# Kernel tuning notes

Hardware: AMD Instinct MI355X
Metric: run time of the kernel (lower is better)

## Reference

```python
import jax, jax.numpy as jnp
import numpy as np

B, T, C, H = 4, 4096, 1024, 64

def setup_inputs() -> dict:
    key = jax.random.key(0)
    kx, kq, kk, kv = jax.random.split(key, 4)
    x = jax.random.normal(kx, (B, T, C), dtype=jnp.float32)
    Wq = jax.random.normal(kq, (C, H), dtype=jnp.float32) * (C ** -0.5)
    Wk = jax.random.normal(kk, (C, H), dtype=jnp.float32) * (C ** -0.5)
    Wv = jax.random.normal(kv, (C, H), dtype=jnp.float32) * (C ** -0.5)
    return {"x": x, "Wq": Wq, "Wk": Wk, "Wv": Wv}

def reference(x, Wq, Wk, Wv):
    # single-head causal attention, dropout p=0 (eval)
    q = jnp.einsum('btc,ch->bth', x, Wq)  # [B,T,H]
    k = jnp.einsum('btc,ch->bth', x, Wk)
    v = jnp.einsum('btc,ch->bth', x, Wv)
    scale = k.shape[-1] ** -0.5
    scores = jnp.einsum('bth,bsh->bts', q, k) * scale  # [B,T,T]
    causal = jnp.tril(jnp.ones((q.shape[1], q.shape[1]), dtype=bool))
    scores = jnp.where(causal, scores, -jnp.inf)
    weights = jax.nn.softmax(scores, axis=-1)
    out = jnp.einsum('bts,bsh->bth', weights, v)  # [B,T,H]
    return out
```

## Files before the change

kernel.cpp:

```cpp
#include <hip/hip_runtime.h>


typedef short  s16x8 __attribute__((ext_vector_type(8)));
typedef float  f32x4 __attribute__((ext_vector_type(4)));

constexpr int B = 4, T = 4096, C = 1024, H = 64;
constexpr int M = B * T;
constexpr float LOG2E = 1.44269504088896340736f;
constexpr float QSCALE = 0.125f * LOG2E;
constexpr float MBASE  = 4.0f * LOG2E;

__device__ __forceinline__ unsigned short f2bf(float f) {
    union { float f; unsigned u; } v; v.f = f;
    unsigned r = v.u + 0x7fffu + ((v.u >> 16) & 1u);
    return (unsigned short)(r >> 16);
}

__device__ __forceinline__ unsigned cvt_pk_bf16(float lo, float hi) {
    unsigned r;
    asm("v_cvt_pk_bf16_f32 %0, %1, %2" : "=v"(r) : "v"(lo), "v"(hi));
    return r;
}

__device__ __forceinline__ void gl_lds16(const void* g, void* l) {
    __builtin_amdgcn_global_load_lds(
        (const __attribute__((address_space(1))) unsigned*)g,
        (__attribute__((address_space(3))) unsigned*)l, 16, 0, 0);
}

__global__ void prep_w(const float* __restrict__ Wq, const float* __restrict__ Wk,
                       const float* __restrict__ Wv, unsigned short* __restrict__ Wt) {
    const int n = blockIdx.x;
    const float* W = (n < 64) ? Wq : (n < 128 ? Wk : Wv);
    const int col = n & 63;
    for (int k = threadIdx.x; k < C; k += blockDim.x)
        Wt[(size_t)n * C + k] = f2bf(W[(size_t)k * H + col]);
}

__global__ __launch_bounds__(512) void qkv_proj(
    const float* __restrict__ x, const unsigned short* __restrict__ Wt,
    unsigned short* __restrict__ Q, unsigned short* __restrict__ K,
    unsigned short* __restrict__ V) {
    __shared__ __align__(16) unsigned short ldsA[2][32 * 64];
    __shared__ __align__(16) unsigned short ldsB[2][192 * 64];

    const int t = threadIdx.x, lane = t & 63, w = t >> 6;
    const int i = lane & 15, g = lane >> 4;
    const int rowbase = blockIdx.x * 32;
    const int rw = w & 1, nw = w >> 1;

    const int arow = t >> 3, aslot = t & 7;
    const float* aga = x + (size_t)(rowbase + arow) * C + ((aslot ^ (arow & 7)) * 8);
    const int awoff = arow * 64 + aslot * 8;
    const bool astage = (t < 256);

    const int brow8 = lane >> 3, bslot = lane & 7;
    const unsigned short* bga[3];
    int bn0[3];
#pragma unroll
    for (int j = 0; j < 3; ++j) {
        bn0[j] = w * 24 + j * 8;
        bga[j] = Wt + (size_t)(bn0[j] + brow8) * C + ((bslot ^ brow8) * 8);
    }

    f32x4 acc[3];
#pragma unroll
    for (int n = 0; n < 3; ++n) acc[n] = (f32x4){0.f, 0.f, 0.f, 0.f};

    {
#pragma unroll
        for (int j = 0; j < 3; ++j)
            gl_lds16(bga[j], &ldsB[0][bn0[j] * 64]);
        if (astage) {
            f32x4 a0 = *(const f32x4*)(aga);
            f32x4 a1 = *(const f32x4*)(aga + 4);
            union { unsigned u[4]; s16x8 v; } av;
            av.u[0] = cvt_pk_bf16(a0[0], a0[1]);
            av.u[1] = cvt_pk_bf16(a0[2], a0[3]);
            av.u[2] = cvt_pk_bf16(a1[0], a1[1]);
            av.u[3] = cvt_pk_bf16(a1[2], a1[3]);
            *(s16x8*)&ldsA[0][awoff] = av.v;
        }
    }
    __syncthreads();

    for (int it = 0; it < 16; ++it) {
        const int cur = it & 1, nxt = cur ^ 1;
        const int kc = (it + 1) * 64;
        f32x4 a0, a1;
        const bool more = (it < 15);
        if (more) {
            if (astage) {
                a0 = *(const f32x4*)(aga + kc);
                a1 = *(const f32x4*)(aga + kc + 4);
            }
#pragma unroll
            for (int j = 0; j < 3; ++j)
                gl_lds16(bga[j] + kc, &ldsB[nxt][bn0[j] * 64]);
        }
#pragma unroll
        for (int kst = 0; kst < 2; ++kst) {
            const int c = kst * 4 + g;
            s16x8 a = *(const s16x8*)&ldsA[cur][(rw * 16 + i) * 64 + ((c ^ (i & 7)) * 8)];
#pragma unroll
            for (int nt = 0; nt < 3; ++nt) {
                int n = nw * 48 + nt * 16 + i;
                s16x8 b = *(const s16x8*)&ldsB[cur][n * 64 + ((c ^ (i & 7)) * 8)];
                acc[nt] = __builtin_amdgcn_mfma_f32_16x16x32_bf16(a, b, acc[nt], 0, 0, 0);
            }
        }
        if (more && astage) {
            union { unsigned u[4]; s16x8 v; } av;
            av.u[0] = cvt_pk_bf16(a0[0], a0[1]);
            av.u[1] = cvt_pk_bf16(a0[2], a0[3]);
            av.u[2] = cvt_pk_bf16(a1[0], a1[1]);
            av.u[3] = cvt_pk_bf16(a1[2], a1[3]);
            *(s16x8*)&ldsA[nxt][awoff] = av.v;
        }
        __syncthreads();
    }

#pragma unroll
    for (int nt = 0; nt < 3; ++nt) {
        int n = nw * 48 + nt * 16 + i;
#pragma unroll
        for (int r = 0; r < 4; ++r) {
            int row = rowbase + rw * 16 + g * 4 + r;
            float val = acc[nt][r];
            if (n < 64)       Q[(size_t)row * H + n]         = f2bf(val * QSCALE);
            else if (n < 128) K[(size_t)row * H + (n - 64)]  = f2bf(val);
            else              V[(size_t)row * H + (n - 128)] = f2bf(val);
        }
    }
}

__global__ __launch_bounds__(256) void vtrans(const unsigned short* __restrict__ V,
                                              unsigned short* __restrict__ VT) {
    __shared__ __align__(16) unsigned short tile[64][72];
    const int b = blockIdx.x >> 6, t0 = (blockIdx.x & 63) * 64;
    const int tid = threadIdx.x;
    {
        int row = tid >> 2, col = (tid & 3) * 16;
        s16x8 v0 = *(const s16x8*)(V + (size_t)(b * T + t0 + row) * H + col);
        s16x8 v1 = *(const s16x8*)(V + (size_t)(b * T + t0 + row) * H + col + 8);
        *(s16x8*)&tile[row][col]     = v0;
        *(s16x8*)&tile[row][col + 8] = v1;
    }
    __syncthreads();
    {
        int h = tid >> 2, tcol = (tid & 3) * 16;
        s16x8 o0, o1;
#pragma unroll
        for (int j = 0; j < 8; ++j) {
            int pos = tcol + j, c = pos >> 5, pp = pos & 31;
            int tok = (c << 5) | (((pp >> 2) & 1) << 4) | ((pp >> 3) << 2) | (pp & 3);
            o0[j] = (short)tile[tok][h];
        }
#pragma unroll
        for (int j = 0; j < 8; ++j) {
            int pos = tcol + 8 + j, c = pos >> 5, pp = pos & 31;
            int tok = (c << 5) | (((pp >> 2) & 1) << 4) | ((pp >> 3) << 2) | (pp & 3);
            o1[j] = (short)tile[tok][h];
        }
        unsigned short* dst = VT + (size_t)(b * H + h) * T + t0 + tcol;
        *(s16x8*)dst       = o0;
        *(s16x8*)(dst + 8) = o1;
    }
}

__global__ __launch_bounds__(256) void attn(
    const unsigned short* __restrict__ Qg, const unsigned short* __restrict__ Kg,
    const unsigned short* __restrict__ VTg,
    float* __restrict__ Opart, float* __restrict__ lpart) {
    __shared__ __align__(16) unsigned short ks[2][64 * 64];
    __shared__ __align__(16) unsigned short vs[2][64 * 64];

    const int t = threadIdx.x, lane = t & 63, w = t >> 6;
    const int bid = blockIdx.x;
    const int xcd3 = bid & 7;
    const int b = xcd3 >> 1, s0 = xcd3 & 1;
    const int rest = bid >> 3;
    const int qgi = rest >> 1, s1 = rest & 1;
    const int sp = s1 * 2 + s0;
    const int qg = 63 - qgi;
    const int q0w = qg * 64 + w * 16;
    const int i = lane & 15, g = lane >> 4, g4 = g * 4;
    const int nkv = qg + 1;

    const unsigned short* Kb = Kg  + (size_t)b * T * H;
    const unsigned short* Vb = VTg + (size_t)b * H * T;

    const int r8 = lane >> 3, sl = lane & 7, sx = sl ^ r8;

    const unsigned short* Qrow = Qg + (size_t)(b * T + q0w + i) * H;
    s16x8 bq0 = *(const s16x8*)(Qrow + g * 8);
    s16x8 bq1 = *(const s16x8*)(Qrow + 32 + g * 8);

    f32x4 oacc[4];
#pragma unroll
    for (int nt = 0; nt < 4; ++nt) oacc[nt] = (f32x4){0.f, 0.f, 0.f, 0.f};
    float l_run = 0.f;

    if (sp < nkv) {
        const int kv0 = sp * 64;
#pragma unroll
        for (int j = 0; j < 2; ++j) {
            const int row = (w + j * 4) * 8 + r8;
            gl_lds16(Kb + (size_t)(kv0 + row) * H + sx * 8, &ks[0][row * 64 + sl * 8]);
            gl_lds16(Vb + (size_t)row * T + kv0 + sx * 8,   &vs[0][row * 64 + sl * 8]);
        }
    }
    __syncthreads();

    int cur = 0;
    for (int tile = sp; tile < nkv; tile += 4) {
        const int kv = tile * 64;
        if (tile + 4 < nkv) {
            const int kvn = kv + 256;
#pragma unroll
            for (int j = 0; j < 2; ++j) {
                const int row = (w + j * 4) * 8 + r8;
                gl_lds16(Kb + (size_t)(kvn + row) * H + sx * 8, &ks[cur ^ 1][row * 64 + sl * 8]);
                gl_lds16(Vb + (size_t)row * T + kvn + sx * 8,   &vs[cur ^ 1][row * 64 + sl * 8]);
            }
        }

        s16x8 kb[8], vb[8];
#pragma unroll
        for (int kst = 0; kst < 2; ++kst)
#pragma unroll
            for (int nt = 0; nt < 4; ++nt) {
                const int off = (nt * 16 + i) * 64 + (((kst * 4 + g) ^ (i & 7)) * 8);
                kb[kst * 4 + nt] = *(const s16x8*)&ks[cur][off];
                vb[kst * 4 + nt] = *(const s16x8*)&vs[cur][off];
            }

        f32x4 s[4];
#pragma unroll
        for (int nt = 0; nt < 4; ++nt)
            s[nt] = (f32x4){-MBASE, -MBASE, -MBASE, -MBASE};
#pragma unroll
        for (int nt = 0; nt < 4; ++nt)
            s[nt] = __builtin_amdgcn_mfma_f32_16x16x32_bf16(kb[nt], bq0, s[nt], 0, 0, 0);
#pragma unroll
        for (int nt = 0; nt < 4; ++nt)
            s[nt] = __builtin_amdgcn_mfma_f32_16x16x32_bf16(kb[4 + nt], bq1, s[nt], 0, 0, 0);

        if (kv + 63 > q0w) {
            const int thr = q0w + i - kv;
#pragma unroll
            for (int nt = 0; nt < 4; ++nt)
#pragma unroll
                for (int r = 0; r < 4; ++r)
                    if (nt * 16 + g4 + r > thr) s[nt][r] = -INFINITY;
        }

#pragma unroll
        for (int nt = 0; nt < 4; ++nt)
#pragma unroll
            for (int r = 0; r < 4; ++r)
                s[nt][r] = exp2f(s[nt][r]);

#pragma unroll
        for (int kst = 0; kst < 2; ++kst) {
            union { unsigned u[4]; s16x8 v; } pb;
            pb.u[0] = cvt_pk_bf16(s[2 * kst][0],     s[2 * kst][1]);
            pb.u[1] = cvt_pk_bf16(s[2 * kst][2],     s[2 * kst][3]);
            pb.u[2] = cvt_pk_bf16(s[2 * kst + 1][0], s[2 * kst + 1][1]);
            pb.u[3] = cvt_pk_bf16(s[2 * kst + 1][2], s[2 * kst + 1][3]);
#pragma unroll
            for (int nt = 0; nt < 4; ++nt)
                oacc[nt] = __builtin_amdgcn_mfma_f32_16x16x32_bf16(vb[kst * 4 + nt], pb.v, oacc[nt], 0, 0, 0);
        }

        l_run += ((s[0][0] + s[0][1]) + (s[0][2] + s[0][3]))
               + ((s[1][0] + s[1][1]) + (s[1][2] + s[1][3]))
               + ((s[2][0] + s[2][1]) + (s[2][2] + s[2][3]))
               + ((s[3][0] + s[3][1]) + (s[3][2] + s[3][3]));

        __syncthreads();
        cur ^= 1;
    }

    l_run += __shfl_xor(l_run, 16);
    l_run += __shfl_xor(l_run, 32);
#pragma unroll
    for (int nt = 0; nt < 4; ++nt)
        *(f32x4*)&Opart[((size_t)bid * 64 + w * 16 + i) * 64 + nt * 16 + g4] = oacc[nt];
    if (g == 0) lpart[(size_t)bid * 64 + w * 16 + i] = l_run;
}

__global__ __launch_bounds__(256) void merge4(
    const float* __restrict__ Opart, const float* __restrict__ lpart,
    float* __restrict__ out) {
    const int idx = blockIdx.x * 256 + threadIdx.x;
    const int row = idx >> 4, c4 = (idx & 15) * 4;
    const int b = row >> 12, q = row & 4095;
    const int qg = q >> 6, r = q & 63;
    const int qgi = 63 - qg;

    float L = 0.f;
    f32x4 o = (f32x4){0.f, 0.f, 0.f, 0.f};
#pragma unroll
    for (int s = 0; s < 4; ++s) {
        const int bidp = ((qgi * 2 + (s >> 1)) << 3) + b * 2 + (s & 1);
        L += lpart[(size_t)bidp * 64 + r];
        f32x4 ov = *(const f32x4*)&Opart[((size_t)bidp * 64 + r) * 64 + c4];
        o[0] += ov[0]; o[1] += ov[1]; o[2] += ov[2]; o[3] += ov[3];
    }
    const float inv = 1.0f / L;
    f32x4 res = (f32x4){o[0] * inv, o[1] * inv, o[2] * inv, o[3] * inv};
    *(f32x4*)&out[(size_t)row * 64 + c4] = res;
}

extern "C" void kernel_launch(void* const* d_in, const int* in_sizes, int n_in,
                              void* d_out, int out_size, void* d_ws, size_t ws_size,
                              hipStream_t stream) {
    (void)in_sizes; (void)n_in; (void)out_size; (void)ws_size;
    const float* x  = (const float*)d_in[0];
    const float* Wq = (const float*)d_in[1];
    const float* Wk = (const float*)d_in[2];
    const float* Wv = (const float*)d_in[3];
    float* out = (float*)d_out;

    char* ws = (char*)d_ws;
    unsigned short* Q  = (unsigned short*)(ws);
    unsigned short* K  = (unsigned short*)(ws + (size_t)1 * M * H * 2);
    unsigned short* V  = (unsigned short*)(ws + (size_t)2 * M * H * 2);
    unsigned short* VT = (unsigned short*)(ws + (size_t)3 * M * H * 2);
    unsigned short* Wt = (unsigned short*)(ws + (size_t)4 * M * H * 2);
    float* Opart = (float*)(ws + (size_t)4 * M * H * 2 + 512 * 1024);
    float* lpart = (float*)(ws + (size_t)4 * M * H * 2 + 512 * 1024
                            + (size_t)1024 * 64 * 64 * 4);

    prep_w<<<192, 256, 0, stream>>>(Wq, Wk, Wv, Wt);
    qkv_proj<<<M / 32, 512, 0, stream>>>(x, Wt, Q, K, V);
    vtrans<<<B * (T / 64), 256, 0, stream>>>(V, VT);
    attn<<<1024, 256, 0, stream>>>(Q, K, VT, Opart, lpart);
    merge4<<<1024, 256, 0, stream>>>(Opart, lpart, out);
}
```

Measured before the change: 55.76 us.

## Use 128-row query tiles with 8-way KV split and bf16 partial outputs

The attention kernel now runs 512-thread blocks covering 128 query rows, so each K/V tile staged in LDS is shared by 8 waves instead of 4. The KV dimension is split 8 ways instead of 4, and waves skip tiles that lie entirely above their causal diagonal. Partial outputs are stored as bf16 instead of fp32, which halves the traffic between the attention and merge kernels. The merge now reads eight partials per row, and the bf16 partials lose some precision before normalization.

```diff
diff --git a/kernel.cpp b/kernel.cpp
--- a/kernel.cpp
+++ b/kernel.cpp
@@ -3,6 +3,7 @@
 
 typedef short  s16x8 __attribute__((ext_vector_type(8)));
 typedef float  f32x4 __attribute__((ext_vector_type(4)));
+typedef unsigned u32x2 __attribute__((ext_vector_type(2)));
 
 constexpr int B = 4, T = 4096, C = 1024, H = 64;
 constexpr int M = B * T;
@@ -168,29 +169,30 @@
     }
 }
 
-__global__ __launch_bounds__(256) void attn(
+__global__ __launch_bounds__(512, 4) void attn(
     const unsigned short* __restrict__ Qg, const unsigned short* __restrict__ Kg,
     const unsigned short* __restrict__ VTg,
-    float* __restrict__ Opart, float* __restrict__ lpart) {
+    unsigned short* __restrict__ Opb, float* __restrict__ lpart) {
     __shared__ __align__(16) unsigned short ks[2][64 * 64];
     __shared__ __align__(16) unsigned short vs[2][64 * 64];
 
     const int t = threadIdx.x, lane = t & 63, w = t >> 6;
     const int bid = blockIdx.x;
-    const int xcd3 = bid & 7;
-    const int b = xcd3 >> 1, s0 = xcd3 & 1;
-    const int rest = bid >> 3;
-    const int qgi = rest >> 1, s1 = rest & 1;
-    const int sp = s1 * 2 + s0;
-    const int qg = 63 - qgi;
-    const int q0w = qg * 64 + w * 16;
+    const int b = bid & 3;
+    const int sp = (bid >> 2) & 7;
+    const int qt = 31 - (bid >> 5);
+    const int q0 = qt * 128;
+    const int q0w = q0 + w * 16;
     const int i = lane & 15, g = lane >> 4, g4 = g * 4;
-    const int nkv = qg + 1;
+    const int nkv = 2 * qt + 2;
 
     const unsigned short* Kb = Kg  + (size_t)b * T * H;
     const unsigned short* Vb = VTg + (size_t)b * H * T;
 
-    const int r8 = lane >> 3, sl = lane & 7, sx = sl ^ r8;
+    const int srow = t >> 3, sl = t & 7, sx = sl ^ (srow & 7);
+    const unsigned short* kga = Kb + (size_t)srow * H + sx * 8;
+    const unsigned short* vga = Vb + (size_t)srow * T + sx * 8;
+    const int soff = srow * 64 + sl * 8;
 
     const unsigned short* Qrow = Qg + (size_t)(b * T + q0w + i) * H;
     s16x8 bq0 = *(const s16x8*)(Qrow + g * 8);
@@ -202,81 +204,75 @@
     float l_run = 0.f;
 
     if (sp < nkv) {
-        const int kv0 = sp * 64;
-#pragma unroll
-        for (int j = 0; j < 2; ++j) {
-            const int row = (w + j * 4) * 8 + r8;
-            gl_lds16(Kb + (size_t)(kv0 + row) * H + sx * 8, &ks[0][row * 64 + sl * 8]);
-            gl_lds16(Vb + (size_t)row * T + kv0 + sx * 8,   &vs[0][row * 64 + sl * 8]);
-        }
+        const size_t kv0 = (size_t)sp * 64;
+        gl_lds16(kga + kv0 * H, &ks[0][soff]);
+        gl_lds16(vga + kv0,     &vs[0][soff]);
     }
     __syncthreads();
 
     int cur = 0;
-    for (int tile = sp; tile < nkv; tile += 4) {
+    for (int tile = sp; tile < nkv; tile += 8) {
         const int kv = tile * 64;
-        if (tile + 4 < nkv) {
-            const int kvn = kv + 256;
-#pragma unroll
-            for (int j = 0; j < 2; ++j) {
-                const int row = (w + j * 4) * 8 + r8;
-                gl_lds16(Kb + (size_t)(kvn + row) * H + sx * 8, &ks[cur ^ 1][row * 64 + sl * 8]);
-                gl_lds16(Vb + (size_t)row * T + kvn + sx * 8,   &vs[cur ^ 1][row * 64 + sl * 8]);
+        if (tile + 8 < nkv) {
+            const size_t kvn = (size_t)kv + 512;
+            gl_lds16(kga + kvn * H, &ks[cur ^ 1][soff]);
+            gl_lds16(vga + kvn,     &vs[cur ^ 1][soff]);
+        }
+
+        if (kv <= q0w + 15) {
+            s16x8 kb[8], vb[8];
+#pragma unroll
+            for (int kst = 0; kst < 2; ++kst)
+#pragma unroll
+                for (int nt = 0; nt < 4; ++nt) {
+                    const int off = (nt * 16 + i) * 64 + (((kst * 4 + g) ^ (i & 7)) * 8);
+                    kb[kst * 4 + nt] = *(const s16x8*)&ks[cur][off];
+                    vb[kst * 4 + nt] = *(const s16x8*)&vs[cur][off];
+                }
+
+            f32x4 s[4];
+#pragma unroll
+            for (int nt = 0; nt < 4; ++nt)
+                s[nt] = (f32x4){-MBASE, -MBASE, -MBASE, -MBASE};
+#pragma unroll
+            for (int nt = 0; nt < 4; ++nt)
+                s[nt] = __builtin_amdgcn_mfma_f32_16x16x32_bf16(kb[nt], bq0, s[nt], 0, 0, 0);
+#pragma unroll
+            for (int nt = 0; nt < 4; ++nt)
+                s[nt] = __builtin_amdgcn_mfma_f32_16x16x32_bf16(kb[4 + nt], bq1, s[nt], 0, 0, 0);
+
+            if (kv + 63 > q0w) {
+                const int thr = q0w + i - kv;
+#pragma unroll
+                for (int nt = 0; nt < 4; ++nt)
+#pragma unroll
+                    for (int r = 0; r < 4; ++r)
+                        if (nt * 16 + g4 + r > thr) s[nt][r] = -INFINITY;
             }
-        }
-
-        s16x8 kb[8], vb[8];
-#pragma unroll
-        for (int kst = 0; kst < 2; ++kst)
-#pragma unroll
-            for (int nt = 0; nt < 4; ++nt) {
-                const int off = (nt * 16 + i) * 64 + (((kst * 4 + g) ^ (i & 7)) * 8);
-                kb[kst * 4 + nt] = *(const s16x8*)&ks[cur][off];
-                vb[kst * 4 + nt] = *(const s16x8*)&vs[cur][off];
+
+#pragma unroll
+            for (int nt = 0; nt < 4; ++nt)
+#pragma unroll
+                for (int r = 0; r < 4; ++r)
+                    s[nt][r] = exp2f(s[nt][r]);
+
+#pragma unroll
+            for (int kst = 0; kst < 2; ++kst) {
+                union { unsigned u[4]; s16x8 v; } pb;
+                pb.u[0] = cvt_pk_bf16(s[2 * kst][0],     s[2 * kst][1]);
+                pb.u[1] = cvt_pk_bf16(s[2 * kst][2],     s[2 * kst][3]);
+                pb.u[2] = cvt_pk_bf16(s[2 * kst + 1][0], s[2 * kst + 1][1]);
+                pb.u[3] = cvt_pk_bf16(s[2 * kst + 1][2], s[2 * kst + 1][3]);
+#pragma unroll
+                for (int nt = 0; nt < 4; ++nt)
+                    oacc[nt] = __builtin_amdgcn_mfma_f32_16x16x32_bf16(vb[kst * 4 + nt], pb.v, oacc[nt], 0, 0, 0);
             }
 
-        f32x4 s[4];
-#pragma unroll
-        for (int nt = 0; nt < 4; ++nt)
-            s[nt] = (f32x4){-MBASE, -MBASE, -MBASE, -MBASE};
-#pragma unroll
-        for (int nt = 0; nt < 4; ++nt)
-            s[nt] = __builtin_amdgcn_mfma_f32_16x16x32_bf16(kb[nt], bq0, s[nt], 0, 0, 0);
-#pragma unroll
-        for (int nt = 0; nt < 4; ++nt)
-            s[nt] = __builtin_amdgcn_mfma_f32_16x16x32_bf16(kb[4 + nt], bq1, s[nt], 0, 0, 0);
-
-        if (kv + 63 > q0w) {
-            const int thr = q0w + i - kv;
-#pragma unroll
-            for (int nt = 0; nt < 4; ++nt)
-#pragma unroll
-                for (int r = 0; r < 4; ++r)
-                    if (nt * 16 + g4 + r > thr) s[nt][r] = -INFINITY;
-        }
-
-#pragma unroll
-        for (int nt = 0; nt < 4; ++nt)
-#pragma unroll
-            for (int r = 0; r < 4; ++r)
-                s[nt][r] = exp2f(s[nt][r]);
-
-#pragma unroll
-        for (int kst = 0; kst < 2; ++kst) {
-            union { unsigned u[4]; s16x8 v; } pb;
-            pb.u[0] = cvt_pk_bf16(s[2 * kst][0],     s[2 * kst][1]);
-            pb.u[1] = cvt_pk_bf16(s[2 * kst][2],     s[2 * kst][3]);
-            pb.u[2] = cvt_pk_bf16(s[2 * kst + 1][0], s[2 * kst + 1][1]);
-            pb.u[3] = cvt_pk_bf16(s[2 * kst + 1][2], s[2 * kst + 1][3]);
-#pragma unroll
-            for (int nt = 0; nt < 4; ++nt)
-                oacc[nt] = __builtin_amdgcn_mfma_f32_16x16x32_bf16(vb[kst * 4 + nt], pb.v, oacc[nt], 0, 0, 0);
-        }
-
-        l_run += ((s[0][0] + s[0][1]) + (s[0][2] + s[0][3]))
-               + ((s[1][0] + s[1][1]) + (s[1][2] + s[1][3]))
-               + ((s[2][0] + s[2][1]) + (s[2][2] + s[2][3]))
-               + ((s[3][0] + s[3][1]) + (s[3][2] + s[3][3]));
+            l_run += ((s[0][0] + s[0][1]) + (s[0][2] + s[0][3]))
+                   + ((s[1][0] + s[1][1]) + (s[1][2] + s[1][3]))
+                   + ((s[2][0] + s[2][1]) + (s[2][2] + s[2][3]))
+                   + ((s[3][0] + s[3][1]) + (s[3][2] + s[3][3]));
+        }
 
         __syncthreads();
         cur ^= 1;
@@ -284,29 +280,40 @@
 
     l_run += __shfl_xor(l_run, 16);
     l_run += __shfl_xor(l_run, 32);
-#pragma unroll
-    for (int nt = 0; nt < 4; ++nt)
-        *(f32x4*)&Opart[((size_t)bid * 64 + w * 16 + i) * 64 + nt * 16 + g4] = oacc[nt];
-    if (g == 0) lpart[(size_t)bid * 64 + w * 16 + i] = l_run;
-}
-
-__global__ __launch_bounds__(256) void merge4(
-    const float* __restrict__ Opart, const float* __restrict__ lpart,
+    unsigned short* op = Opb + ((size_t)bid * 128 + w * 16 + i) * 64;
+#pragma unroll
+    for (int nt = 0; nt < 4; ++nt) {
+        u32x2 pk;
+        pk[0] = cvt_pk_bf16(oacc[nt][0], oacc[nt][1]);
+        pk[1] = cvt_pk_bf16(oacc[nt][2], oacc[nt][3]);
+        *(u32x2*)(op + nt * 16 + g4) = pk;
+    }
+    if (g == 0) lpart[(size_t)bid * 128 + w * 16 + i] = l_run;
+}
+
+__global__ __launch_bounds__(256) void merge8(
+    const unsigned short* __restrict__ Opb, const float* __restrict__ lpart,
     float* __restrict__ out) {
     const int idx = blockIdx.x * 256 + threadIdx.x;
     const int row = idx >> 4, c4 = (idx & 15) * 4;
     const int b = row >> 12, q = row & 4095;
-    const int qg = q >> 6, r = q & 63;
-    const int qgi = 63 - qg;
+    const int qt = q >> 7, r = q & 127;
+    const int qti = 31 - qt;
 
     float L = 0.f;
     f32x4 o = (f32x4){0.f, 0.f, 0.f, 0.f};
 #pragma unroll
-    for (int s = 0; s < 4; ++s) {
-        const int bidp = ((qgi * 2 + (s >> 1)) << 3) + b * 2 + (s & 1);
-        L += lpart[(size_t)bidp * 64 + r];
-        f32x4 ov = *(const f32x4*)&Opart[((size_t)bidp * 64 + r) * 64 + c4];
-        o[0] += ov[0]; o[1] += ov[1]; o[2] += ov[2]; o[3] += ov[3];
+    for (int sp = 0; sp < 8; ++sp) {
+        const int bidp = qti * 32 + sp * 4 + b;
+        L += lpart[(size_t)bidp * 128 + r];
+        union { unsigned long long d; unsigned short s[4]; } v;
+        v.d = *(const unsigned long long*)&Opb[((size_t)bidp * 128 + r) * 64 + c4];
+#pragma unroll
+        for (int k = 0; k < 4; ++k) {
+            union { unsigned u; float f; } cv;
+            cv.u = (unsigned)v.s[k] << 16;
+            o[k] += cv.f;
+        }
     }
     const float inv = 1.0f / L;
     f32x4 res = (f32x4){o[0] * inv, o[1] * inv, o[2] * inv, o[3] * inv};
@@ -329,13 +336,13 @@
     unsigned short* V  = (unsigned short*)(ws + (size_t)2 * M * H * 2);
     unsigned short* VT = (unsigned short*)(ws + (size_t)3 * M * H * 2);
     unsigned short* Wt = (unsigned short*)(ws + (size_t)4 * M * H * 2);
-    float* Opart = (float*)(ws + (size_t)4 * M * H * 2 + 512 * 1024);
+    unsigned short* Opb = (unsigned short*)(ws + (size_t)4 * M * H * 2 + 512 * 1024);
     float* lpart = (float*)(ws + (size_t)4 * M * H * 2 + 512 * 1024
-                            + (size_t)1024 * 64 * 64 * 4);
+                            + (size_t)1024 * 128 * 64 * 2);
 
     prep_w<<<192, 256, 0, stream>>>(Wq, Wk, Wv, Wt);
     qkv_proj<<<M / 32, 512, 0, stream>>>(x, Wt, Q, K, V);
     vtrans<<<B * (T / 64), 256, 0, stream>>>(V, VT);
-    attn<<<1024, 256, 0, stream>>>(Q, K, VT, Opart, lpart);
-    merge4<<<1024, 256, 0, stream>>>(Opart, lpart, out);
-}
+    attn<<<1024, 512, 0, stream>>>(Q, K, VT, Opb, lpart);
+    merge8<<<1024, 256, 0, stream>>>(Opb, lpart, out);
+}
```

New measurement: 55.56 us. No clear change (-0.4%).
